# Kernel tuning notes

Measured on AMD Instinct MI355X. Metric: run time of the kernel, lower is better.

## Reference

```python
import jax, jax.numpy as jnp
import numpy as np


def setup_inputs() -> dict:
    key = jax.random.key(0)
    ks = jax.random.split(key, 6)
    N, E, D = 50000, 400000, 128
    x = jax.random.normal(ks[0], (N, D), dtype=jnp.float32)
    edge_attr = jax.random.normal(ks[1], (E, D), dtype=jnp.float32)
    edge_index = jax.random.randint(ks[2], (2, E), 0, N, dtype=jnp.int64)
    # LatentMLP: two linear layers (3*D -> D -> D) with ReLU activations
    W1 = jax.random.normal(ks[3], (3 * D, D), dtype=jnp.float32) * (1.0 / np.sqrt(3 * D))
    b1 = jnp.zeros((D,), dtype=jnp.float32)
    W2 = jax.random.normal(ks[4], (D, D), dtype=jnp.float32) * (1.0 / np.sqrt(D))
    b2 = jnp.zeros((D,), dtype=jnp.float32)
    return {"x": x, "edge_attr": edge_attr, "edge_index": edge_index,
            "W1": W1, "b1": b1, "W2": W2, "b2": b2}


def reference(x, edge_attr, edge_index, W1, b1, W2, b2):
    src, dst = edge_index[0], edge_index[1]
    # gather node features per edge: [E, D] each
    agg = jnp.concatenate([x[src], x[dst], edge_attr], axis=1)  # [E, 3D]
    h = jax.nn.relu(agg @ W1 + b1)   # [E, D]
    out = jax.nn.relu(h @ W2 + b2)   # [E, D] -> new edge_attr
    return out
```

## Files before the change

kernel.cpp:

```cpp
#include <hip/hip_runtime.h>
#include <hip/hip_bf16.h>

typedef __bf16 bf16_t;
typedef __bf16 bf16x8 __attribute__((ext_vector_type(8)));
typedef __bf16 bf16x4 __attribute__((ext_vector_type(4)));
typedef float  f32x4  __attribute__((ext_vector_type(4)));

#define D  128
#define BM 128

__device__ __forceinline__ int swz(int r, int c) {
    return (r * D + c) ^ ((r & 7) << 3);
}

__global__ void prep_weights_kernel(const float* __restrict__ W1,
                                    const float* __restrict__ W2,
                                    bf16_t* __restrict__ ws) {
    int t = blockIdx.x * 256 + threadIdx.x;
    int s = t >> 14, r = t & 16383;
    int n = r >> 7, k = r & 127;
    float v = (s < 3) ? W1[(s * 128 + k) * 128 + n] : W2[k * 128 + n];
    ws[t] = (bf16_t)v;
}

__global__ __launch_bounds__(256, 2)
void fused_edge_mlp_kernel(const float* __restrict__ x,
                           const float* __restrict__ ea,
                           const int* __restrict__ ei,
                           const bf16_t* __restrict__ ws,
                           const float* __restrict__ b1,
                           const float* __restrict__ b2,
                           float* __restrict__ out,
                           int E) {
    __shared__ __align__(16) bf16_t Ab[BM * D];
    __shared__ __align__(16) bf16_t Bb[D * D];

    const int tid  = threadIdx.x;
    const int lane = tid & 63;
    const int wv   = tid >> 6;
    const int col0 = lane & 15;
    const int krow = lane >> 4;
    const int l31  = lane & 31;
    const int half = lane >> 5;
    const int e0   = blockIdx.x * BM;

    const int erL  = min(e0 + wv * 32 + l31, E - 1);
    const int sidx = ei[erL];
    const int didx = ei[E + erL];

    const int brow_t = tid >> 4;
    const int bslot  = (tid & 15) * 8;

    f32x4  abuf[16];
    bf16x8 bnext[8];

    {
        const bf16_t* base = ws;
#pragma unroll
        for (int j = 0; j < 8; j++)
            bnext[j] = *(const bf16x8*)(base + (j * 16 + brow_t) * 128 + bslot);
    }
#pragma unroll
    for (int j = 0; j < 16; j++) {
        int r = j * 2 + half;
        int g = __shfl(sidx, r);
        abuf[j] = *(const f32x4*)(x + (long long)g * D + l31 * 4);
    }

    float bias1[8], bias2[8];
#pragma unroll
    for (int n = 0; n < 8; n++) { bias1[n] = b1[n*16 + col0]; bias2[n] = b2[n*16 + col0]; }

#pragma unroll
    for (int j = 0; j < 8; j++)
        *(bf16x8*)&Bb[swz(j * 16 + brow_t, bslot)] = bnext[j];
#pragma unroll
    for (int j = 0; j < 16; j++) {
        int r = j * 2 + half;
        f32x4 v = abuf[j];
        bf16x4 hv = { (bf16_t)v.x, (bf16_t)v.y, (bf16_t)v.z, (bf16_t)v.w };
        *(bf16x4*)&Ab[swz(wv * 32 + r, l31 * 4)] = hv;
    }
    __syncthreads();

    f32x4 acc[2][8];
#pragma unroll
    for (int m = 0; m < 2; m++)
#pragma unroll
        for (int n = 0; n < 8; n++) acc[m][n] = (f32x4){0.f, 0.f, 0.f, 0.f};

#pragma unroll
    for (int p = 0; p < 4; p++) {
        if (p < 3) {
            const bf16_t* base = ws + (p + 1) * 16384;
#pragma unroll
            for (int j = 0; j < 8; j++)
                bnext[j] = *(const bf16x8*)(base + (j * 16 + brow_t) * 128 + bslot);
        }
        if (p < 2) {
#pragma unroll
            for (int j = 0; j < 16; j++) {
                int r = j * 2 + half;
                const float* rp;
                if (p == 0) { int g = __shfl(didx, r); rp = x + (long long)g * D; }
                else        { int e = min(e0 + wv * 32 + r, E - 1); rp = ea + (long long)e * D; }
                abuf[j] = *(const f32x4*)(rp + l31 * 4);
            }
        }

#pragma unroll
        for (int kk = 0; kk < 4; kk++) {
            bf16x8 a0 = *(const bf16x8*)&Ab[swz(wv*32 +      col0, kk*32 + krow*8)];
            bf16x8 a1 = *(const bf16x8*)&Ab[swz(wv*32 + 16 + col0, kk*32 + krow*8)];
#pragma unroll
            for (int n = 0; n < 8; n++) {
                bf16x8 b = *(const bf16x8*)&Bb[swz(n*16 + col0, kk*32 + krow*8)];
                acc[0][n] = __builtin_amdgcn_mfma_f32_16x16x32_bf16(a0, b, acc[0][n], 0, 0, 0);
                acc[1][n] = __builtin_amdgcn_mfma_f32_16x16x32_bf16(a1, b, acc[1][n], 0, 0, 0);
            }
        }

        if (p < 2) {
#pragma unroll
            for (int j = 0; j < 16; j++) {
                int r = j * 2 + half;
                f32x4 v = abuf[j];
                bf16x4 hv = { (bf16_t)v.x, (bf16_t)v.y, (bf16_t)v.z, (bf16_t)v.w };
                *(bf16x4*)&Ab[swz(wv * 32 + r, l31 * 4)] = hv;
            }
        }
        if (p == 2) {
#pragma unroll
            for (int m = 0; m < 2; m++)
#pragma unroll
                for (int n = 0; n < 8; n++)
#pragma unroll
                    for (int ri = 0; ri < 4; ri++) {
                        float hv = fmaxf(acc[m][n][ri] + bias1[n], 0.f);
                        Ab[swz(wv*32 + m*16 + krow*4 + ri, n*16 + col0)] = (bf16_t)hv;
                    }
#pragma unroll
            for (int m = 0; m < 2; m++)
#pragma unroll
                for (int n = 0; n < 8; n++) acc[m][n] = (f32x4){0.f, 0.f, 0.f, 0.f};
        }
        if (p < 3) {
            __syncthreads();
#pragma unroll
            for (int j = 0; j < 8; j++)
                *(bf16x8*)&Bb[swz(j * 16 + brow_t, bslot)] = bnext[j];
            __syncthreads();
        }
    }

#pragma unroll
    for (int m = 0; m < 2; m++)
#pragma unroll
        for (int n = 0; n < 8; n++)
#pragma unroll
            for (int ri = 0; ri < 4; ri++) {
                int row = wv*32 + m*16 + krow*4 + ri;
                int e = e0 + row;
                if (e < E) out[(long long)e * D + n*16 + col0] = fmaxf(acc[m][n][ri] + bias2[n], 0.f);
            }
}

extern "C" void kernel_launch(void* const* d_in, const int* in_sizes, int n_in,
                              void* d_out, int out_size, void* d_ws, size_t ws_size,
                              hipStream_t stream) {
    const float* x  = (const float*)d_in[0];
    const float* ea = (const float*)d_in[1];
    const int*   ei = (const int*)d_in[2];
    const float* W1 = (const float*)d_in[3];
    const float* b1 = (const float*)d_in[4];
    const float* W2 = (const float*)d_in[5];
    const float* b2 = (const float*)d_in[6];
    float* out = (float*)d_out;

    const int E = in_sizes[1] / D;

    bf16_t* wsl = (bf16_t*)d_ws;

    prep_weights_kernel<<<256, 256, 0, stream>>>(W1, W2, wsl);

    int nblocks = (E + BM - 1) / BM;
    fused_edge_mlp_kernel<<<nblocks, 256, 0, stream>>>(x, ea, ei, wsl, b1, b2, out, E);
}
```

Before: 144.2 us.

## Precompute per-node projections and gather them per edge instead of raw features

The first linear layer is split algebraically: x@W1a and x@W1b are computed once per node (N=50k) in a new uv_kernel and stored as bf16. The edge kernel then gathers these precomputed projections and only multiplies edge_attr by the third W1 block. This removes two thirds of the per-edge first-layer matmul and halves the gather bytes by using bf16. It adds a node-level pass, extra workspace traffic, and extra bf16 rounding of u and v and of their sum. Blocks also grow to 512 threads with 128KB of dynamic LDS.

```diff
diff --git a/kernel.cpp b/kernel.cpp
--- a/kernel.cpp
+++ b/kernel.cpp
@@ -6,8 +6,8 @@
 typedef __bf16 bf16x4 __attribute__((ext_vector_type(4)));
 typedef float  f32x4  __attribute__((ext_vector_type(4)));
 
-#define D  128
-#define BM 128
+#define D 128
+#define LDS_BYTES 131072
 
 __device__ __forceinline__ int swz(int r, int c) {
     return (r * D + c) ^ ((r & 7) << 3);
@@ -23,133 +23,184 @@
     ws[t] = (bf16_t)v;
 }
 
-__global__ __launch_bounds__(256, 2)
-void fused_edge_mlp_kernel(const float* __restrict__ x,
-                           const float* __restrict__ ea,
-                           const int* __restrict__ ei,
-                           const bf16_t* __restrict__ ws,
-                           const float* __restrict__ b1,
-                           const float* __restrict__ b2,
-                           float* __restrict__ out,
-                           int E) {
-    __shared__ __align__(16) bf16_t Ab[BM * D];
-    __shared__ __align__(16) bf16_t Bb[D * D];
-
-    const int tid  = threadIdx.x;
-    const int lane = tid & 63;
-    const int wv   = tid >> 6;
-    const int col0 = lane & 15;
-    const int krow = lane >> 4;
-    const int l31  = lane & 31;
-    const int half = lane >> 5;
-    const int e0   = blockIdx.x * BM;
-
-    const int erL  = min(e0 + wv * 32 + l31, E - 1);
-    const int sidx = ei[erL];
-    const int didx = ei[E + erL];
-
-    const int brow_t = tid >> 4;
-    const int bslot  = (tid & 15) * 8;
-
-    f32x4  abuf[16];
-    bf16x8 bnext[8];
-
-    {
-        const bf16_t* base = ws;
-#pragma unroll
-        for (int j = 0; j < 8; j++)
-            bnext[j] = *(const bf16x8*)(base + (j * 16 + brow_t) * 128 + bslot);
-    }
-#pragma unroll
-    for (int j = 0; j < 16; j++) {
-        int r = j * 2 + half;
-        int g = __shfl(sidx, r);
-        abuf[j] = *(const f32x4*)(x + (long long)g * D + l31 * 4);
-    }
-
-    float bias1[8], bias2[8];
-#pragma unroll
-    for (int n = 0; n < 8; n++) { bias1[n] = b1[n*16 + col0]; bias2[n] = b2[n*16 + col0]; }
-
-#pragma unroll
-    for (int j = 0; j < 8; j++)
-        *(bf16x8*)&Bb[swz(j * 16 + brow_t, bslot)] = bnext[j];
-#pragma unroll
-    for (int j = 0; j < 16; j++) {
-        int r = j * 2 + half;
-        f32x4 v = abuf[j];
-        bf16x4 hv = { (bf16_t)v.x, (bf16_t)v.y, (bf16_t)v.z, (bf16_t)v.w };
-        *(bf16x4*)&Ab[swz(wv * 32 + r, l31 * 4)] = hv;
+__global__ __launch_bounds__(512, 2)
+void uv_kernel(const float* __restrict__ x, const bf16_t* __restrict__ ws,
+               const float* __restrict__ b1, bf16_t* __restrict__ u,
+               bf16_t* __restrict__ v, int N) {
+    extern __shared__ __align__(16) bf16_t lds[];
+    const int tid = threadIdx.x, lane = tid & 63, wv = tid >> 6;
+    const int col0 = lane & 15, krow = lane >> 4, l31 = lane & 31, half = lane >> 5;
+    const int gr = lane >> 4, gc = (lane & 15) * 8;
+    const int n0 = blockIdx.x * 256 + wv * 32;
+    bf16_t* Ach = lds + 32768 + wv * 4096;
+
+    f32x4 xb[16];
+#pragma unroll
+    for (int j = 0; j < 16; j++) {
+        int node = min(n0 + j * 2 + half, N - 1);
+        xb[j] = *(const f32x4*)(x + (long long)node * D + l31 * 4);
+    }
+#pragma unroll
+    for (int s = 0; s < 2; s++)
+#pragma unroll
+        for (int j = 0; j < 4; j++) {
+            int row = j * 32 + (tid >> 4), slot = (tid & 15) * 8;
+            bf16x8 w = *(const bf16x8*)(ws + s * 16384 + row * 128 + slot);
+            *(bf16x8*)&lds[s * 16384 + swz(row, slot)] = w;
+        }
+    float bias1[8];
+#pragma unroll
+    for (int n = 0; n < 8; n++) bias1[n] = b1[n * 16 + col0];
+#pragma unroll
+    for (int j = 0; j < 16; j++) {
+        f32x4 vv = xb[j];
+        bf16x4 hv = { (bf16_t)vv.x, (bf16_t)vv.y, (bf16_t)vv.z, (bf16_t)vv.w };
+        *(bf16x4*)&Ach[swz(j * 2 + half, l31 * 4)] = hv;
     }
     __syncthreads();
 
+    f32x4 aU[2][8], aV[2][8];
+#pragma unroll
+    for (int m = 0; m < 2; m++)
+#pragma unroll
+        for (int n = 0; n < 8; n++) { aU[m][n] = (f32x4){0,0,0,0}; aV[m][n] = (f32x4){0,0,0,0}; }
+#pragma unroll
+    for (int kk = 0; kk < 4; kk++) {
+        bf16x8 a0 = *(const bf16x8*)&Ach[swz(col0, kk*32 + krow*8)];
+        bf16x8 a1 = *(const bf16x8*)&Ach[swz(16 + col0, kk*32 + krow*8)];
+#pragma unroll
+        for (int n = 0; n < 8; n++) {
+            bf16x8 bU = *(const bf16x8*)&lds[swz(n*16 + col0, kk*32 + krow*8)];
+            bf16x8 bV = *(const bf16x8*)&lds[16384 + swz(n*16 + col0, kk*32 + krow*8)];
+            aU[0][n] = __builtin_amdgcn_mfma_f32_16x16x32_bf16(a0, bU, aU[0][n], 0,0,0);
+            aU[1][n] = __builtin_amdgcn_mfma_f32_16x16x32_bf16(a1, bU, aU[1][n], 0,0,0);
+            aV[0][n] = __builtin_amdgcn_mfma_f32_16x16x32_bf16(a0, bV, aV[0][n], 0,0,0);
+            aV[1][n] = __builtin_amdgcn_mfma_f32_16x16x32_bf16(a1, bV, aV[1][n], 0,0,0);
+        }
+    }
+#pragma unroll
+    for (int m = 0; m < 2; m++)
+#pragma unroll
+        for (int n = 0; n < 8; n++)
+#pragma unroll
+            for (int ri = 0; ri < 4; ri++)
+                Ach[swz(m*16 + krow*4 + ri, n*16 + col0)] = (bf16_t)(aU[m][n][ri] + bias1[n]);
+#pragma unroll
+    for (int j = 0; j < 8; j++) {
+        int r = j * 4 + gr, node = n0 + r;
+        if (node < N) *(bf16x8*)(u + (long long)node * D + gc) = *(const bf16x8*)&Ach[swz(r, gc)];
+    }
+#pragma unroll
+    for (int m = 0; m < 2; m++)
+#pragma unroll
+        for (int n = 0; n < 8; n++)
+#pragma unroll
+            for (int ri = 0; ri < 4; ri++)
+                Ach[swz(m*16 + krow*4 + ri, n*16 + col0)] = (bf16_t)(aV[m][n][ri]);
+#pragma unroll
+    for (int j = 0; j < 8; j++) {
+        int r = j * 4 + gr, node = n0 + r;
+        if (node < N) *(bf16x8*)(v + (long long)node * D + gc) = *(const bf16x8*)&Ach[swz(r, gc)];
+    }
+}
+
+__global__ __launch_bounds__(512, 2)
+void edge_kernel(const bf16_t* __restrict__ u, const bf16_t* __restrict__ v,
+                 const float* __restrict__ ea, const int* __restrict__ ei,
+                 const bf16_t* __restrict__ ws, const float* __restrict__ b2,
+                 float* __restrict__ out, int E) {
+    extern __shared__ __align__(16) bf16_t lds[];
+    const int tid = threadIdx.x, lane = tid & 63, wv = tid >> 6;
+    const int col0 = lane & 15, krow = lane >> 4, l31 = lane & 31, half = lane >> 5;
+    const int gr = lane >> 4, gc = (lane & 15) * 8;
+    const int g0 = blockIdx.x * 256 + wv * 32;
+    bf16_t* Ach = lds + 32768 + wv * 4096;
+
+    const int er = min(g0 + l31, E - 1);
+    const int sidx = ei[er];
+    const int didx = ei[E + er];
+
+    f32x4 eaB[16];
+#pragma unroll
+    for (int j = 0; j < 16; j++) {
+        int e = min(g0 + j * 2 + half, E - 1);
+        eaB[j] = *(const f32x4*)(ea + (long long)e * D + l31 * 4);
+    }
+#pragma unroll
+    for (int s = 0; s < 2; s++)
+#pragma unroll
+        for (int j = 0; j < 4; j++) {
+            int row = j * 32 + (tid >> 4), slot = (tid & 15) * 8;
+            bf16x8 w = *(const bf16x8*)(ws + (2 + s) * 16384 + row * 128 + slot);
+            *(bf16x8*)&lds[s * 16384 + swz(row, slot)] = w;
+        }
+    float bias2[8];
+#pragma unroll
+    for (int n = 0; n < 8; n++) bias2[n] = b2[n * 16 + col0];
+#pragma unroll
+    for (int j = 0; j < 16; j++) {
+        f32x4 vv = eaB[j];
+        bf16x4 hv = { (bf16_t)vv.x, (bf16_t)vv.y, (bf16_t)vv.z, (bf16_t)vv.w };
+        *(bf16x4*)&Ach[swz(j * 2 + half, l31 * 4)] = hv;
+    }
+    __syncthreads();
+
+    bf16x8 bufU[8], bufV[8];
+#pragma unroll
+    for (int j = 0; j < 8; j++) { int gi = __shfl(sidx, j * 4 + gr); bufU[j] = *(const bf16x8*)(u + (long long)gi * D + gc); }
+#pragma unroll
+    for (int j = 0; j < 8; j++) { int gi = __shfl(didx, j * 4 + gr); bufV[j] = *(const bf16x8*)(v + (long long)gi * D + gc); }
+
     f32x4 acc[2][8];
 #pragma unroll
     for (int m = 0; m < 2; m++)
 #pragma unroll
-        for (int n = 0; n < 8; n++) acc[m][n] = (f32x4){0.f, 0.f, 0.f, 0.f};
-
-#pragma unroll
-    for (int p = 0; p < 4; p++) {
-        if (p < 3) {
-            const bf16_t* base = ws + (p + 1) * 16384;
-#pragma unroll
-            for (int j = 0; j < 8; j++)
-                bnext[j] = *(const bf16x8*)(base + (j * 16 + brow_t) * 128 + bslot);
-        }
-        if (p < 2) {
-#pragma unroll
-            for (int j = 0; j < 16; j++) {
-                int r = j * 2 + half;
-                const float* rp;
-                if (p == 0) { int g = __shfl(didx, r); rp = x + (long long)g * D; }
-                else        { int e = min(e0 + wv * 32 + r, E - 1); rp = ea + (long long)e * D; }
-                abuf[j] = *(const f32x4*)(rp + l31 * 4);
+        for (int n = 0; n < 8; n++) acc[m][n] = (f32x4){0,0,0,0};
+
+#pragma unroll
+    for (int kk = 0; kk < 4; kk++) {
+        bf16x8 a0 = *(const bf16x8*)&Ach[swz(col0, kk*32 + krow*8)];
+        bf16x8 a1 = *(const bf16x8*)&Ach[swz(16 + col0, kk*32 + krow*8)];
+#pragma unroll
+        for (int n = 0; n < 8; n++) {
+            bf16x8 b = *(const bf16x8*)&lds[swz(n*16 + col0, kk*32 + krow*8)];
+            acc[0][n] = __builtin_amdgcn_mfma_f32_16x16x32_bf16(a0, b, acc[0][n], 0,0,0);
+            acc[1][n] = __builtin_amdgcn_mfma_f32_16x16x32_bf16(a1, b, acc[1][n], 0,0,0);
+        }
+    }
+
+#pragma unroll
+    for (int j = 0; j < 8; j++) {
+        bf16x8 su = bufU[j], sv = bufV[j], sr;
+#pragma unroll
+        for (int t = 0; t < 8; t++) sr[t] = (bf16_t)((float)su[t] + (float)sv[t]);
+        *(bf16x8*)&Ach[swz(j * 4 + gr, gc)] = sr;
+    }
+#pragma unroll
+    for (int m = 0; m < 2; m++)
+#pragma unroll
+        for (int n = 0; n < 8; n++)
+#pragma unroll
+            for (int ri = 0; ri < 4; ri++) {
+                int row = m*16 + krow*4 + ri, col = n*16 + col0;
+                float sval = (float)Ach[swz(row, col)];
+                float hv = fmaxf(acc[m][n][ri] + sval, 0.f);
+                Ach[swz(row, col)] = (bf16_t)hv;
             }
-        }
-
-#pragma unroll
-        for (int kk = 0; kk < 4; kk++) {
-            bf16x8 a0 = *(const bf16x8*)&Ab[swz(wv*32 +      col0, kk*32 + krow*8)];
-            bf16x8 a1 = *(const bf16x8*)&Ab[swz(wv*32 + 16 + col0, kk*32 + krow*8)];
-#pragma unroll
-            for (int n = 0; n < 8; n++) {
-                bf16x8 b = *(const bf16x8*)&Bb[swz(n*16 + col0, kk*32 + krow*8)];
-                acc[0][n] = __builtin_amdgcn_mfma_f32_16x16x32_bf16(a0, b, acc[0][n], 0, 0, 0);
-                acc[1][n] = __builtin_amdgcn_mfma_f32_16x16x32_bf16(a1, b, acc[1][n], 0, 0, 0);
-            }
-        }
-
-        if (p < 2) {
-#pragma unroll
-            for (int j = 0; j < 16; j++) {
-                int r = j * 2 + half;
-                f32x4 v = abuf[j];
-                bf16x4 hv = { (bf16_t)v.x, (bf16_t)v.y, (bf16_t)v.z, (bf16_t)v.w };
-                *(bf16x4*)&Ab[swz(wv * 32 + r, l31 * 4)] = hv;
-            }
-        }
-        if (p == 2) {
-#pragma unroll
-            for (int m = 0; m < 2; m++)
-#pragma unroll
-                for (int n = 0; n < 8; n++)
-#pragma unroll
-                    for (int ri = 0; ri < 4; ri++) {
-                        float hv = fmaxf(acc[m][n][ri] + bias1[n], 0.f);
-                        Ab[swz(wv*32 + m*16 + krow*4 + ri, n*16 + col0)] = (bf16_t)hv;
-                    }
-#pragma unroll
-            for (int m = 0; m < 2; m++)
-#pragma unroll
-                for (int n = 0; n < 8; n++) acc[m][n] = (f32x4){0.f, 0.f, 0.f, 0.f};
-        }
-        if (p < 3) {
-            __syncthreads();
-#pragma unroll
-            for (int j = 0; j < 8; j++)
-                *(bf16x8*)&Bb[swz(j * 16 + brow_t, bslot)] = bnext[j];
-            __syncthreads();
+#pragma unroll
+    for (int m = 0; m < 2; m++)
+#pragma unroll
+        for (int n = 0; n < 8; n++) acc[m][n] = (f32x4){0,0,0,0};
+
+#pragma unroll
+    for (int kk = 0; kk < 4; kk++) {
+        bf16x8 a0 = *(const bf16x8*)&Ach[swz(col0, kk*32 + krow*8)];
+        bf16x8 a1 = *(const bf16x8*)&Ach[swz(16 + col0, kk*32 + krow*8)];
+#pragma unroll
+        for (int n = 0; n < 8; n++) {
+            bf16x8 b = *(const bf16x8*)&lds[16384 + swz(n*16 + col0, kk*32 + krow*8)];
+            acc[0][n] = __builtin_amdgcn_mfma_f32_16x16x32_bf16(a0, b, acc[0][n], 0,0,0);
+            acc[1][n] = __builtin_amdgcn_mfma_f32_16x16x32_bf16(a1, b, acc[1][n], 0,0,0);
         }
     }
 
@@ -159,8 +210,7 @@
         for (int n = 0; n < 8; n++)
 #pragma unroll
             for (int ri = 0; ri < 4; ri++) {
-                int row = wv*32 + m*16 + krow*4 + ri;
-                int e = e0 + row;
+                int e = g0 + m*16 + krow*4 + ri;
                 if (e < E) out[(long long)e * D + n*16 + col0] = fmaxf(acc[m][n][ri] + bias2[n], 0.f);
             }
 }
@@ -178,11 +228,20 @@
     float* out = (float*)d_out;
 
     const int E = in_sizes[1] / D;
+    const int N = in_sizes[0] / D;
 
     bf16_t* wsl = (bf16_t*)d_ws;
+    bf16_t* uu  = wsl + 4 * 16384;
+    bf16_t* vv  = uu + (size_t)N * D;
 
     prep_weights_kernel<<<256, 256, 0, stream>>>(W1, W2, wsl);
 
-    int nblocks = (E + BM - 1) / BM;
-    fused_edge_mlp_kernel<<<nblocks, 256, 0, stream>>>(x, ea, ei, wsl, b1, b2, out, E);
-}
+    hipFuncSetAttribute(reinterpret_cast<const void*>(uv_kernel),
+                        hipFuncAttributeMaxDynamicSharedMemorySize, LDS_BYTES);
+    hipFuncSetAttribute(reinterpret_cast<const void*>(edge_kernel),
+                        hipFuncAttributeMaxDynamicSharedMemorySize, LDS_BYTES);
+
+    uv_kernel<<<(N + 255) / 256, 512, LDS_BYTES, stream>>>(x, wsl, b1, uu, vv, N);
+
+    edge_kernel<<<(E + 255) / 256, 512, LDS_BYTES, stream>>>(uu, vv, ea, ei, wsl, b2, out, E);
+}
```

Measured after the change: 150.1 us. +4.1%, slower.
